# Optimization experiments

Hardware: AMD Instinct MI355X
Metric: run time of the kernel (lower is better)

The kernel has to match this reference:

```python
import jax, jax.numpy as jnp
import numpy as np

N_NODES = 200000
N_ELEMS = 400000
NNPE = 8   # nodes per element (hex8)
NQ = 8     # quadrature points
ND = 3     # spatial dim
NDOF = 3   # field components


def setup_inputs() -> dict:
    key = jax.random.key(0)
    ks = jax.random.split(key, 8)
    coords = jax.random.uniform(ks[0], (N_NODES, ND), dtype=jnp.float32)
    # small displacements so det(I + grad_u) > 0
    us = 0.01 * jax.random.normal(ks[1], (N_NODES, NDOF), dtype=jnp.float32)
    shape_vals = jax.random.uniform(ks[2], (NQ, NNPE), dtype=jnp.float32)
    shape_grads = 0.1 * jax.random.normal(ks[3], (NQ, NNPE, ND), dtype=jnp.float32)
    JxWs = jax.random.uniform(ks[4], (N_ELEMS, NQ), dtype=jnp.float32)
    conns = jax.random.randint(ks[5], (N_ELEMS, NNPE), 0, N_NODES, dtype=jnp.int64)
    params = jnp.ones((2,), dtype=jnp.float32)  # (mu, lambda)
    t = jax.random.uniform(ks[6], (1,), dtype=jnp.float32)
    dt = jnp.ones((1,), dtype=jnp.float32)
    state_old = jnp.zeros((N_ELEMS, NQ, 1), dtype=jnp.float32)
    return {"params": params, "coords": coords, "t": t, "us": us,
            "shape_vals": shape_vals, "shape_grads": shape_grads,
            "JxWs": JxWs, "dt": dt, "state_old": state_old, "conns": conns}


def _neo_hookean_energy(mu, lam, grad_uq):
    # grad_uq: [E, Q, ndof, nd]
    F = grad_uq + jnp.eye(ND, dtype=grad_uq.dtype)          # deformation gradient
    J = jnp.linalg.det(F)                                    # [E, Q]
    I1 = jnp.einsum('eqij,eqij->eq', F, F)                   # tr(F^T F)
    logJ = jnp.log(J)
    return 0.5 * mu * (I1 - 3.0 - 2.0 * logJ) + 0.5 * lam * logJ * logJ


def reference(params, coords, t, us, shape_vals, shape_grads, JxWs, dt,
              state_old, conns):
    # --- gather nodal data per element (irregular access) ---
    xs_e = coords[conns]   # [E, nnpe, nd]
    us_e = us[conns]       # [E, nnpe, ndof]
    # --- shape-function interpolation (element_interpolants) ---
    xq = jnp.einsum('qn,end->eqd', shape_vals, xs_e)         # quad-pt coords
    uq = jnp.einsum('qn,enf->eqf', shape_vals, us_e)         # quad-pt fields
    grad_uq = jnp.einsum('qnd,enf->eqfd', shape_grads, us_e)  # [E,Q,ndof,nd]
    # --- vmapped energy at each quadrature point ---
    mu, lam = params[0], params[1]
    fs = _neo_hookean_energy(mu, lam, grad_uq)               # [E, Q]
    state_new = state_old                                    # state pass-through
    # --- quadrature-weighted reduce, then sum over elements ---
    pis = jnp.sum(JxWs * fs, axis=1)                         # [E]
    pi = jnp.sum(pis)
    return pi, state_new
```

## Files before the change

### kernel.cpp

```cpp
#include <hip/hip_runtime.h>

#define N_ELEMS_C 400000
#define N_NODES_C 200000
#define STATE_N   3200000
#define N_BLOCKS  ((N_ELEMS_C + 255) / 256)

#define WS_PARTIALS_OFF (4 * 1024 * 1024)

typedef float v4f __attribute__((ext_vector_type(4)));
typedef int   v4i __attribute__((ext_vector_type(4)));


__global__ __launch_bounds__(256) void repack_us_kernel(
    const float* __restrict__ us, v4f* __restrict__ usw)
{
    const int t = blockIdx.x * 256 + threadIdx.x;
    if (t < N_NODES_C / 4) {
        const v4f* src = reinterpret_cast<const v4f*>(us);
        const v4f a = __builtin_nontemporal_load(src + 3 * t + 0);
        const v4f b = __builtin_nontemporal_load(src + 3 * t + 1);
        const v4f c = __builtin_nontemporal_load(src + 3 * t + 2);
        usw[4 * t + 0] = (v4f){a.x, a.y, a.z, 0.f};
        usw[4 * t + 1] = (v4f){a.w, b.x, b.y, 0.f};
        usw[4 * t + 2] = (v4f){b.z, b.w, c.x, 0.f};
        usw[4 * t + 3] = (v4f){c.y, c.z, c.w, 0.f};
    }
}

__global__ __launch_bounds__(256) void fused_energy_kernel(
    const float* __restrict__ params,
    const v4f* __restrict__ usw,
    const float* __restrict__ shape_grads,
    const float* __restrict__ jxws,
    const int*   __restrict__ conns,
    const float* __restrict__ state_old,
    float* __restrict__ partials,
    float* __restrict__ out)
{
    __shared__ __align__(16) float s_sgT[192];
    __shared__ float s_wsum[4];
    const int tid = threadIdx.x;
    const int b   = blockIdx.x;

    if (tid < 192) {
        const int q = tid / 24;
        const int r = tid % 24;
        const int d = r / 8;
        const int n = r % 8;
        s_sgT[tid] = shape_grads[(q * 8 + n) * 3 + d];
    }

    {
        const int base4 = b * 512;
        #pragma unroll
        for (int k = 0; k < 2; ++k) {
            const int i4 = base4 + k * 256 + tid;
            if (i4 < STATE_N / 4) {
                const v4f v = __builtin_nontemporal_load(
                    reinterpret_cast<const v4f*>(state_old) + i4);
                const int i = i4 * 4;
                __builtin_nontemporal_store(v.x, out + 1 + i + 0);
                __builtin_nontemporal_store(v.y, out + 1 + i + 1);
                __builtin_nontemporal_store(v.z, out + 1 + i + 2);
                __builtin_nontemporal_store(v.w, out + 1 + i + 3);
            }
        }
    }

    __syncthreads();

    const int e = b * 256 + tid;
    float acc = 0.0f;
    if (e < N_ELEMS_C) {
        const float mu  = params[0];
        const float lam = params[1];

        const v4i* cp = reinterpret_cast<const v4i*>(conns);
        const v4i c0 = __builtin_nontemporal_load(cp + 2 * e + 0);
        const v4i c1 = __builtin_nontemporal_load(cp + 2 * e + 1);
        const int ci[8] = {c0.x, c0.y, c0.z, c0.w, c1.x, c1.y, c1.z, c1.w};

        v4f uv[8];
        #pragma unroll
        for (int n = 0; n < 8; ++n) uv[n] = usw[ci[n]];

        const v4f* jp = reinterpret_cast<const v4f*>(jxws);
        const v4f j0 = __builtin_nontemporal_load(jp + 2 * e + 0);
        const v4f j1 = __builtin_nontemporal_load(jp + 2 * e + 1);
        const float jq[8] = {j0.x, j0.y, j0.z, j0.w, j1.x, j1.y, j1.z, j1.w};

        #pragma unroll
        for (int q = 0; q < 8; ++q) {
            const v4f* sgq = reinterpret_cast<const v4f*>(s_sgT + q * 24);
            const v4f A0 = sgq[0], A1 = sgq[1];
            const v4f B0 = sgq[2], B1 = sgq[3];
            const v4f C0 = sgq[4], C1 = sgq[5];
            const float d0[8] = {A0.x, A0.y, A0.z, A0.w, A1.x, A1.y, A1.z, A1.w};
            const float d1[8] = {B0.x, B0.y, B0.z, B0.w, B1.x, B1.y, B1.z, B1.w};
            const float d2[8] = {C0.x, C0.y, C0.z, C0.w, C1.x, C1.y, C1.z, C1.w};

            float g00=0.f,g01=0.f,g02=0.f,g10=0.f,g11=0.f,g12=0.f,g20=0.f,g21=0.f,g22=0.f;
            #pragma unroll
            for (int n = 0; n < 8; ++n) {
                const float u0 = uv[n].x, u1 = uv[n].y, u2 = uv[n].z;
                g00 = fmaf(d0[n], u0, g00); g01 = fmaf(d1[n], u0, g01); g02 = fmaf(d2[n], u0, g02);
                g10 = fmaf(d0[n], u1, g10); g11 = fmaf(d1[n], u1, g11); g12 = fmaf(d2[n], u1, g12);
                g20 = fmaf(d0[n], u2, g20); g21 = fmaf(d1[n], u2, g21); g22 = fmaf(d2[n], u2, g22);
            }
            const float F00 = g00 + 1.0f, F01 = g01,        F02 = g02;
            const float F10 = g10,        F11 = g11 + 1.0f, F12 = g12;
            const float F20 = g20,        F21 = g21,        F22 = g22 + 1.0f;

            const float det = F00 * (F11 * F22 - F12 * F21)
                            - F01 * (F10 * F22 - F12 * F20)
                            + F02 * (F10 * F21 - F11 * F20);
            const float I1 = F00*F00 + F01*F01 + F02*F02
                           + F10*F10 + F11*F11 + F12*F12
                           + F20*F20 + F21*F21 + F22*F22;
            const float lj = __logf(det);
            const float fq = 0.5f * mu * (I1 - 3.0f - 2.0f * lj)
                           + 0.5f * lam * lj * lj;
            acc = fmaf(jq[q], fq, acc);
        }
    }

    #pragma unroll
    for (int off = 32; off > 0; off >>= 1)
        acc += __shfl_down(acc, off, 64);
    const int lane = tid & 63;
    const int wv   = tid >> 6;
    if (lane == 0) s_wsum[wv] = acc;
    __syncthreads();
    if (tid == 0) {
        partials[b] = s_wsum[0] + s_wsum[1] + s_wsum[2] + s_wsum[3];
    }
}

__global__ __launch_bounds__(256) void final_reduce_kernel(
    const float* __restrict__ partials, float* __restrict__ out)
{
    __shared__ float s_wsum[4];
    const int tid = threadIdx.x;
    float acc = 0.0f;
    for (int i = tid; i < N_BLOCKS; i += 256) acc += partials[i];
    #pragma unroll
    for (int off = 32; off > 0; off >>= 1)
        acc += __shfl_down(acc, off, 64);
    const int lane = tid & 63;
    const int wv   = tid >> 6;
    if (lane == 0) s_wsum[wv] = acc;
    __syncthreads();
    if (tid == 0) {
        out[0] = s_wsum[0] + s_wsum[1] + s_wsum[2] + s_wsum[3];
    }
}

extern "C" void kernel_launch(void* const* d_in, const int* in_sizes, int n_in,
                              void* d_out, int out_size, void* d_ws, size_t ws_size,
                              hipStream_t stream) {
    const float* params      = (const float*)d_in[0];
    const float* us          = (const float*)d_in[3];
    const float* shape_grads = (const float*)d_in[5];
    const float* jxws        = (const float*)d_in[6];
    const float* state_old   = (const float*)d_in[8];
    const int*   conns       = (const int*)d_in[9];
    float* out      = (float*)d_out;
    v4f* usw        = (v4f*)d_ws;
    float* partials = (float*)((char*)d_ws + WS_PARTIALS_OFF);

    hipLaunchKernelGGL(repack_us_kernel,
                       dim3((N_NODES_C / 4 + 255) / 256), dim3(256), 0, stream,
                       us, usw);
    hipLaunchKernelGGL(fused_energy_kernel,
                       dim3(N_BLOCKS), dim3(256), 0, stream,
                       params, usw, shape_grads, jxws, conns, state_old,
                       partials, out);
    hipLaunchKernelGGL(final_reduce_kernel,
                       dim3(1), dim3(256), 0, stream,
                       partials, out);
}
```

Before: 128.4 us.

## Drop us repack kernel and fuse final reduction via last-block atomic counter

Removes the separate kernel that padded the node displacements to 16-byte records. The energy kernel now gathers directly from the packed 12-byte-stride array using unaligned 4-float loads. The separate final-reduce launch is replaced by a last-block-done pattern: a global atomic counter, reset by a memset, selects the block that sums all partials. This saves a kernel launch and an extra pass over the displacement data. In exchange, unaligned gathers can straddle cache lines more often, the load for the last node reads one float past the end of the array, and the memset adds a small operation of its own.

```diff
diff --git a/kernel.cpp b/kernel.cpp
--- a/kernel.cpp
+++ b/kernel.cpp
@@ -5,40 +5,26 @@
 #define STATE_N   3200000
 #define N_BLOCKS  ((N_ELEMS_C + 255) / 256)
 
-#define WS_PARTIALS_OFF (4 * 1024 * 1024)
+#define WS_PARTIALS_OFF 256
 
 typedef float v4f __attribute__((ext_vector_type(4)));
 typedef int   v4i __attribute__((ext_vector_type(4)));
 
-
-__global__ __launch_bounds__(256) void repack_us_kernel(
-    const float* __restrict__ us, v4f* __restrict__ usw)
-{
-    const int t = blockIdx.x * 256 + threadIdx.x;
-    if (t < N_NODES_C / 4) {
-        const v4f* src = reinterpret_cast<const v4f*>(us);
-        const v4f a = __builtin_nontemporal_load(src + 3 * t + 0);
-        const v4f b = __builtin_nontemporal_load(src + 3 * t + 1);
-        const v4f c = __builtin_nontemporal_load(src + 3 * t + 2);
-        usw[4 * t + 0] = (v4f){a.x, a.y, a.z, 0.f};
-        usw[4 * t + 1] = (v4f){a.w, b.x, b.y, 0.f};
-        usw[4 * t + 2] = (v4f){b.z, b.w, c.x, 0.f};
-        usw[4 * t + 3] = (v4f){c.y, c.z, c.w, 0.f};
-    }
-}
-
 __global__ __launch_bounds__(256) void fused_energy_kernel(
     const float* __restrict__ params,
-    const v4f* __restrict__ usw,
+    const float* __restrict__ us,
     const float* __restrict__ shape_grads,
     const float* __restrict__ jxws,
     const int*   __restrict__ conns,
     const float* __restrict__ state_old,
     float* __restrict__ partials,
+    int*   __restrict__ counter,
     float* __restrict__ out)
 {
     __shared__ __align__(16) float s_sgT[192];
     __shared__ float s_wsum[4];
+    __shared__ float s_wsum2[4];
+    __shared__ int   s_last;
     const int tid = threadIdx.x;
     const int b   = blockIdx.x;
 
@@ -82,7 +68,8 @@
 
         v4f uv[8];
         #pragma unroll
-        for (int n = 0; n < 8; ++n) uv[n] = usw[ci[n]];
+        for (int n = 0; n < 8; ++n)
+            uv[n] = *reinterpret_cast<const v4f*>(us + 3 * (size_t)ci[n]);
 
         const v4f* jp = reinterpret_cast<const v4f*>(jxws);
         const v4f j0 = __builtin_nontemporal_load(jp + 2 * e + 0);
@@ -133,25 +120,23 @@
     __syncthreads();
     if (tid == 0) {
         partials[b] = s_wsum[0] + s_wsum[1] + s_wsum[2] + s_wsum[3];
+        __threadfence();
+        const int old = atomicAdd(counter, 1);
+        s_last = (old == N_BLOCKS - 1);
     }
-}
+    __syncthreads();
 
-__global__ __launch_bounds__(256) void final_reduce_kernel(
-    const float* __restrict__ partials, float* __restrict__ out)
-{
-    __shared__ float s_wsum[4];
-    const int tid = threadIdx.x;
-    float acc = 0.0f;
-    for (int i = tid; i < N_BLOCKS; i += 256) acc += partials[i];
-    #pragma unroll
-    for (int off = 32; off > 0; off >>= 1)
-        acc += __shfl_down(acc, off, 64);
-    const int lane = tid & 63;
-    const int wv   = tid >> 6;
-    if (lane == 0) s_wsum[wv] = acc;
-    __syncthreads();
-    if (tid == 0) {
-        out[0] = s_wsum[0] + s_wsum[1] + s_wsum[2] + s_wsum[3];
+    if (s_last) {
+        float a2 = 0.0f;
+        for (int i = tid; i < N_BLOCKS; i += 256)
+            a2 += atomicAdd(&partials[i], 0.0f);
+        #pragma unroll
+        for (int off = 32; off > 0; off >>= 1)
+            a2 += __shfl_down(a2, off, 64);
+        if (lane == 0) s_wsum2[wv] = a2;
+        __syncthreads();
+        if (tid == 0)
+            out[0] = s_wsum2[0] + s_wsum2[1] + s_wsum2[2] + s_wsum2[3];
     }
 }
 
@@ -165,17 +150,12 @@
     const float* state_old   = (const float*)d_in[8];
     const int*   conns       = (const int*)d_in[9];
     float* out      = (float*)d_out;
-    v4f* usw        = (v4f*)d_ws;
+    int*   counter  = (int*)d_ws;
     float* partials = (float*)((char*)d_ws + WS_PARTIALS_OFF);
 
-    hipLaunchKernelGGL(repack_us_kernel,
-                       dim3((N_NODES_C / 4 + 255) / 256), dim3(256), 0, stream,
-                       us, usw);
+    hipMemsetAsync(counter, 0, sizeof(int), stream);
     hipLaunchKernelGGL(fused_energy_kernel,
                        dim3(N_BLOCKS), dim3(256), 0, stream,
-                       params, usw, shape_grads, jxws, conns, state_old,
-                       partials, out);
-    hipLaunchKernelGGL(final_reduce_kernel,
-                       dim3(1), dim3(256), 0, stream,
-                       partials, out);
+                       params, us, shape_grads, jxws, conns, state_old,
+                       partials, counter, out);
 }
```

Result: slower. 194.9 us (+51.8%).

## Drop us repack kernel, process two elements per thread with interleaved state copy

Applied to the files above, without the earlier changes.

Removes the separate kernel that padded the displacement array to 16-byte nodes. The energy kernel now gathers nodal displacements straight from the packed xyz array using unaligned 4-float loads. Each thread now handles two elements and four state chunks, and all independent loads are issued before compute and the state stores, to raise memory-level parallelism. This saves a launch and the repack traffic, but the gathers become misaligned, may touch more cache lines, and read one float past the end of the array for the last node. Register pressure per thread also goes up.

```diff
diff --git a/kernel.cpp b/kernel.cpp
--- a/kernel.cpp
+++ b/kernel.cpp
@@ -3,33 +3,16 @@
 #define N_ELEMS_C 400000
 #define N_NODES_C 200000
 #define STATE_N   3200000
-#define N_BLOCKS  ((N_ELEMS_C + 255) / 256)
+#define N_BLOCKS  ((N_ELEMS_C + 511) / 512)
 
-#define WS_PARTIALS_OFF (4 * 1024 * 1024)
+#define WS_PARTIALS_OFF 0
 
 typedef float v4f __attribute__((ext_vector_type(4)));
 typedef int   v4i __attribute__((ext_vector_type(4)));
 
-
-__global__ __launch_bounds__(256) void repack_us_kernel(
-    const float* __restrict__ us, v4f* __restrict__ usw)
-{
-    const int t = blockIdx.x * 256 + threadIdx.x;
-    if (t < N_NODES_C / 4) {
-        const v4f* src = reinterpret_cast<const v4f*>(us);
-        const v4f a = __builtin_nontemporal_load(src + 3 * t + 0);
-        const v4f b = __builtin_nontemporal_load(src + 3 * t + 1);
-        const v4f c = __builtin_nontemporal_load(src + 3 * t + 2);
-        usw[4 * t + 0] = (v4f){a.x, a.y, a.z, 0.f};
-        usw[4 * t + 1] = (v4f){a.w, b.x, b.y, 0.f};
-        usw[4 * t + 2] = (v4f){b.z, b.w, c.x, 0.f};
-        usw[4 * t + 3] = (v4f){c.y, c.z, c.w, 0.f};
-    }
-}
-
 __global__ __launch_bounds__(256) void fused_energy_kernel(
     const float* __restrict__ params,
-    const v4f* __restrict__ usw,
+    const float* __restrict__ us,
     const float* __restrict__ shape_grads,
     const float* __restrict__ jxws,
     const int*   __restrict__ conns,
@@ -49,55 +32,87 @@
         const int n = r % 8;
         s_sgT[tid] = shape_grads[(q * 8 + n) * 3 + d];
     }
+    __syncthreads();
 
-    {
-        const int base4 = b * 512;
+    const int e0 = b * 512 + tid;
+    const int e1 = e0 + 256;
+    const bool a0 = (e0 < N_ELEMS_C), a1 = (e1 < N_ELEMS_C);
+
+    v4i c00={0,0,0,0}, c01={0,0,0,0}, c10={0,0,0,0}, c11={0,0,0,0};
+    v4f j00={0,0,0,0}, j01={0,0,0,0}, j10={0,0,0,0}, j11={0,0,0,0};
+    const v4i* cp = reinterpret_cast<const v4i*>(conns);
+    const v4f* jp = reinterpret_cast<const v4f*>(jxws);
+    if (a0) {
+        c00 = __builtin_nontemporal_load(cp + 2 * e0 + 0);
+        c01 = __builtin_nontemporal_load(cp + 2 * e0 + 1);
+        j00 = __builtin_nontemporal_load(jp + 2 * e0 + 0);
+        j01 = __builtin_nontemporal_load(jp + 2 * e0 + 1);
+    }
+    if (a1) {
+        c10 = __builtin_nontemporal_load(cp + 2 * e1 + 0);
+        c11 = __builtin_nontemporal_load(cp + 2 * e1 + 1);
+        j10 = __builtin_nontemporal_load(jp + 2 * e1 + 0);
+        j11 = __builtin_nontemporal_load(jp + 2 * e1 + 1);
+    }
+
+    const int base4 = b * 1024;
+    v4f sv[4];
+    bool ok[4];
+    #pragma unroll
+    for (int k = 0; k < 4; ++k) {
+        const int i4 = base4 + k * 256 + tid;
+        ok[k] = (i4 < STATE_N / 4);
+        if (ok[k]) sv[k] = __builtin_nontemporal_load(
+                       reinterpret_cast<const v4f*>(state_old) + i4);
+    }
+
+    v4f uv0[8], uv1[8];
+    if (a0) {
+        const int ci[8] = {c00.x, c00.y, c00.z, c00.w, c01.x, c01.y, c01.z, c01.w};
         #pragma unroll
-        for (int k = 0; k < 2; ++k) {
-            const int i4 = base4 + k * 256 + tid;
-            if (i4 < STATE_N / 4) {
-                const v4f v = __builtin_nontemporal_load(
-                    reinterpret_cast<const v4f*>(state_old) + i4);
-                const int i = i4 * 4;
-                __builtin_nontemporal_store(v.x, out + 1 + i + 0);
-                __builtin_nontemporal_store(v.y, out + 1 + i + 1);
-                __builtin_nontemporal_store(v.z, out + 1 + i + 2);
-                __builtin_nontemporal_store(v.w, out + 1 + i + 3);
-            }
+        for (int n = 0; n < 8; ++n)
+            uv0[n] = *reinterpret_cast<const v4f*>(us + 3 * (size_t)ci[n]);
+    }
+    if (a1) {
+        const int ci[8] = {c10.x, c10.y, c10.z, c10.w, c11.x, c11.y, c11.z, c11.w};
+        #pragma unroll
+        for (int n = 0; n < 8; ++n)
+            uv1[n] = *reinterpret_cast<const v4f*>(us + 3 * (size_t)ci[n]);
+    }
+
+    #pragma unroll
+    for (int k = 0; k < 4; ++k) {
+        if (ok[k]) {
+            const int i = (base4 + k * 256 + tid) * 4;
+            __builtin_nontemporal_store(sv[k].x, out + 1 + i + 0);
+            __builtin_nontemporal_store(sv[k].y, out + 1 + i + 1);
+            __builtin_nontemporal_store(sv[k].z, out + 1 + i + 2);
+            __builtin_nontemporal_store(sv[k].w, out + 1 + i + 3);
         }
     }
 
-    __syncthreads();
+    const float mu  = params[0];
+    const float lam = params[1];
+    const float jq0[8] = {j00.x, j00.y, j00.z, j00.w, j01.x, j01.y, j01.z, j01.w};
+    const float jq1[8] = {j10.x, j10.y, j10.z, j10.w, j11.x, j11.y, j11.z, j11.w};
 
-    const int e = b * 256 + tid;
     float acc = 0.0f;
-    if (e < N_ELEMS_C) {
-        const float mu  = params[0];
-        const float lam = params[1];
-
-        const v4i* cp = reinterpret_cast<const v4i*>(conns);
-        const v4i c0 = __builtin_nontemporal_load(cp + 2 * e + 0);
-        const v4i c1 = __builtin_nontemporal_load(cp + 2 * e + 1);
-        const int ci[8] = {c0.x, c0.y, c0.z, c0.w, c1.x, c1.y, c1.z, c1.w};
-
-        v4f uv[8];
-        #pragma unroll
-        for (int n = 0; n < 8; ++n) uv[n] = usw[ci[n]];
-
-        const v4f* jp = reinterpret_cast<const v4f*>(jxws);
-        const v4f j0 = __builtin_nontemporal_load(jp + 2 * e + 0);
-        const v4f j1 = __builtin_nontemporal_load(jp + 2 * e + 1);
-        const float jq[8] = {j0.x, j0.y, j0.z, j0.w, j1.x, j1.y, j1.z, j1.w};
+    #pragma unroll
+    for (int q = 0; q < 8; ++q) {
+        const v4f* sgq = reinterpret_cast<const v4f*>(s_sgT + q * 24);
+        const v4f A0 = sgq[0], A1 = sgq[1];
+        const v4f B0 = sgq[2], B1 = sgq[3];
+        const v4f C0 = sgq[4], C1 = sgq[5];
+        const float d0[8] = {A0.x, A0.y, A0.z, A0.w, A1.x, A1.y, A1.z, A1.w};
+        const float d1[8] = {B0.x, B0.y, B0.z, B0.w, B1.x, B1.y, B1.z, B1.w};
+        const float d2[8] = {C0.x, C0.y, C0.z, C0.w, C1.x, C1.y, C1.z, C1.w};
 
         #pragma unroll
-        for (int q = 0; q < 8; ++q) {
-            const v4f* sgq = reinterpret_cast<const v4f*>(s_sgT + q * 24);
-            const v4f A0 = sgq[0], A1 = sgq[1];
-            const v4f B0 = sgq[2], B1 = sgq[3];
-            const v4f C0 = sgq[4], C1 = sgq[5];
-            const float d0[8] = {A0.x, A0.y, A0.z, A0.w, A1.x, A1.y, A1.z, A1.w};
-            const float d1[8] = {B0.x, B0.y, B0.z, B0.w, B1.x, B1.y, B1.z, B1.w};
-            const float d2[8] = {C0.x, C0.y, C0.z, C0.w, C1.x, C1.y, C1.z, C1.w};
+        for (int el = 0; el < 2; ++el) {
+            const bool act = el ? a1 : a0;
+            if (!act) continue;
+            const v4f* uv = el ? uv1 : uv0;
+            const float jw = el ? jq1[q] : jq0[q];
 
             float g00=0.f,g01=0.f,g02=0.f,g10=0.f,g11=0.f,g12=0.f,g20=0.f,g21=0.f,g22=0.f;
             #pragma unroll
@@ -120,7 +135,7 @@
             const float lj = __logf(det);
             const float fq = 0.5f * mu * (I1 - 3.0f - 2.0f * lj)
                            + 0.5f * lam * lj * lj;
-            acc = fmaf(jq[q], fq, acc);
+            acc = fmaf(jw, fq, acc);
         }
     }
 
@@ -165,15 +180,11 @@
     const float* state_old   = (const float*)d_in[8];
     const int*   conns       = (const int*)d_in[9];
     float* out      = (float*)d_out;
-    v4f* usw        = (v4f*)d_ws;
     float* partials = (float*)((char*)d_ws + WS_PARTIALS_OFF);
 
-    hipLaunchKernelGGL(repack_us_kernel,
-                       dim3((N_NODES_C / 4 + 255) / 256), dim3(256), 0, stream,
-                       us, usw);
     hipLaunchKernelGGL(fused_energy_kernel,
                        dim3(N_BLOCKS), dim3(256), 0, stream,
-                       params, usw, shape_grads, jxws, conns, state_old,
+                       params, us, shape_grads, jxws, conns, state_old,
                        partials, out);
     hipLaunchKernelGGL(final_reduce_kernel,
                        dim3(1), dim3(256), 0, stream,
```

Result: slower. 132.0 us (+2.9%).
